# Kernel optimization log

Hardware: AMD Instinct MI355X
Metric: run time of the kernel (lower is better)

Reference implementation:

```python
import jax, jax.numpy as jnp
import numpy as np

# Winograd F(2x2, 3x3) transform matrices
_BT = np.array([[1, 0, -1, 0],
                [0, 1,  1, 0],
                [0, -1, 1, 0],
                [0, 1,  0, -1]], dtype=np.float32)
_G = np.array([[1.0, 0.0, 0.0],
               [0.5, 0.5, 0.5],
               [0.5, -0.5, 0.5],
               [0.0, 0.0, 1.0]], dtype=np.float32)
_AT = np.array([[1, 1, 1, 0],
                [0, 1, -1, -1]], dtype=np.float32)


def setup_inputs() -> dict:
    key = jax.random.key(0)
    k1, k2, k3 = jax.random.split(key, 3)
    B, Cin, Cout, H, W = 16, 128, 256, 64, 64
    X = jax.random.normal(k1, (B, Cin, H, W), dtype=jnp.float32)
    # kaiming-uniform-ish scale for a 3x3 conv
    fan_in = Cin * 9
    bound = 1.0 / np.sqrt(fan_in)
    weight = jax.random.uniform(k2, (Cout, Cin, 3, 3), dtype=jnp.float32,
                                minval=-bound * np.sqrt(3.0), maxval=bound * np.sqrt(3.0))
    bias = jax.random.uniform(k3, (Cout,), dtype=jnp.float32, minval=-bound, maxval=bound)
    return {"X": X, "weight": weight, "bias": bias}


def reference(X, weight, bias):
    # Winograd F(2x2,3x3) convolution, stride 1, padding 1 ('same').
    BT = jnp.asarray(_BT, X.dtype)
    G = jnp.asarray(_G, X.dtype)
    AT = jnp.asarray(_AT, X.dtype)
    Bn, C, H, W = X.shape
    K = weight.shape[0]
    tH, tW = H // 2, W // 2  # number of 2x2 output tiles per dim

    xp = jnp.pad(X, ((0, 0), (0, 0), (1, 1), (1, 1)))
    # overlapping 4x4 input tiles with stride 2 -> [B, C, tH, tW, 4, 4]
    rows = (jnp.arange(tH) * 2)[:, None] + jnp.arange(4)[None, :]  # [tH,4]
    cols = (jnp.arange(tW) * 2)[:, None] + jnp.arange(4)[None, :]  # [tW,4]
    d = xp[:, :, rows[:, None, :, None], cols[None, :, None, :]]   # [B,C,tH,tW,4,4]

    # input transform V = B^T d B
    V = jnp.einsum('px,bcijxy,qy->bcijpq', BT, d, BT)
    # filter transform U = G g G^T -> [K,C,4,4]
    U = jnp.einsum('px,kcxy,qy->kcpq', G, weight, G)
    # elementwise product in transform domain, contracted over input channels
    M = jnp.einsum('kcpq,bcijpq->bkijpq', U, V)
    # inverse transform Y = A^T M A -> 2x2 output tiles
    Y = jnp.einsum('px,bkijxy,qy->bkijpq', AT, M, AT)  # [B,K,tH,tW,2,2]

    out = Y.transpose(0, 1, 2, 4, 3, 5).reshape(Bn, K, H, W)
    return out + bias[None, :, None, None]
```

## Files before the change

kernel.cpp:

```cpp
#include <hip/hip_runtime.h>
#include <hip/hip_bf16.h>
#include <cstdint>

#define CIN   128
#define COUT  256
#define BATCH 16
#define HH    64
#define WW    64
#define TH    32
#define TW    32
#define NT    (BATCH*TH*TW)
#define APQ   (COUT*CIN)
#define BPQ   (NT*CIN)

typedef __bf16 bf16x8 __attribute__((ext_vector_type(8)));
typedef float  f32x4  __attribute__((ext_vector_type(4)));

__device__ __forceinline__ void gload16(const void* g, void* l) {
    __builtin_amdgcn_global_load_lds(
        (const __attribute__((address_space(1))) uint32_t*)g,
        (__attribute__((address_space(3))) uint32_t*)l, 16, 0, 0);
}

__global__ __launch_bounds__(256) void wg_wtrans(const float* __restrict__ w,
                                                 __hip_bfloat16* __restrict__ U) {
    int idx = blockIdx.x * 256 + threadIdx.x;
    if (idx >= COUT * CIN) return;
    const float* wp = w + idx * 9;
    float g[3][3];
#pragma unroll
    for (int x = 0; x < 3; x++)
#pragma unroll
        for (int y = 0; y < 3; y++) g[x][y] = wp[x * 3 + y];

    float t[4][3];
#pragma unroll
    for (int y = 0; y < 3; y++) {
        t[0][y] = g[0][y];
        t[1][y] = 0.5f * (g[0][y] + g[1][y] + g[2][y]);
        t[2][y] = 0.5f * (g[0][y] - g[1][y] + g[2][y]);
        t[3][y] = g[2][y];
    }
#pragma unroll
    for (int p = 0; p < 4; p++) {
        float u0 = t[p][0];
        float u1 = 0.5f * (t[p][0] + t[p][1] + t[p][2]);
        float u2 = 0.5f * (t[p][0] - t[p][1] + t[p][2]);
        float u3 = t[p][2];
        U[(p * 4 + 0) * APQ + idx] = __float2bfloat16(u0);
        U[(p * 4 + 1) * APQ + idx] = __float2bfloat16(u1);
        U[(p * 4 + 2) * APQ + idx] = __float2bfloat16(u2);
        U[(p * 4 + 3) * APQ + idx] = __float2bfloat16(u3);
    }
}

__global__ __launch_bounds__(1024) void wg_itrans(const float* __restrict__ X,
                                                  __hip_bfloat16* __restrict__ V) {
    __shared__ float lds[32 * 265];
    const int c0 = blockIdx.x * 32;
    const int i  = blockIdx.y;
    const int b  = blockIdx.z;
    const int tid = threadIdx.x;

    for (int t = tid; t < 32 * 4; t += 1024) {
        int cc = t >> 2, r = t & 3;
        lds[cc * 265 + r * 66 + 0]  = 0.f;
        lds[cc * 265 + r * 66 + 65] = 0.f;
    }
    for (int t = tid; t < 32 * 4 * 64; t += 1024) {
        int x = t & 63, r = (t >> 6) & 3, cc = t >> 8;
        int y = 2 * i - 1 + r;
        float v = 0.f;
        if (y >= 0 && y < HH) v = X[(((b * CIN) + (c0 + cc)) * HH + y) * WW + x];
        lds[cc * 265 + r * 66 + 1 + x] = v;
    }
    __syncthreads();

    const int c = tid & 31;
    const int j = tid >> 5;
    const float* base = &lds[c * 265 + 2 * j];

    float t0[4], t1[4], t2[4], t3[4];
#pragma unroll
    for (int y = 0; y < 4; y++) {
        float a  = base[0 * 66 + y];
        float bb = base[1 * 66 + y];
        float cc = base[2 * 66 + y];
        float dd = base[3 * 66 + y];
        t0[y] = a - cc;
        t1[y] = bb + cc;
        t2[y] = cc - bb;
        t3[y] = bb - dd;
    }
    float vm[4][4];
#pragma unroll
    for (int p = 0; p < 4; p++) {
        const float* tp = (p == 0) ? t0 : (p == 1) ? t1 : (p == 2) ? t2 : t3;
        vm[p][0] = tp[0] - tp[2];
        vm[p][1] = tp[1] + tp[2];
        vm[p][2] = tp[2] - tp[1];
        vm[p][3] = tp[1] - tp[3];
    }

    const int bij = b * (TH * TW) + i * TW + j;
    const int vo  = bij * CIN + (c0 + c);
#pragma unroll
    for (int p = 0; p < 4; p++)
#pragma unroll
        for (int q = 0; q < 4; q++)
            V[(size_t)(p * 4 + q) * BPQ + vo] = __float2bfloat16(vm[p][q]);
}

#define ABYTES 16384
#define BUFSZ  32768

__global__ __launch_bounds__(512, 2) void wg_gemm13(const __hip_bfloat16* __restrict__ U,
                                                    const __hip_bfloat16* __restrict__ V,
                                                    const float* __restrict__ bias,
                                                    float* __restrict__ out) {
    __shared__ char lds[4 * BUFSZ];

    int orig = blockIdx.x;
    int wgid = (orig & 7) * 32 + (orig >> 3);
    const int mt = wgid & 1, nt = wgid >> 1;
    const int m0 = mt * 128, n0 = nt * 128;

    const int tid  = threadIdx.x;
    const int lane = tid & 63;
    const int wave = tid >> 6;
    const int wm = wave >> 2, wn = wave & 3;

    const __hip_bfloat16* pa[2];
    const __hip_bfloat16* pb[2];
    int ldsA[2], ldsB[2];
#pragma unroll
    for (int ch = 0; ch < 2; ch++) {
        int c = ch * 512 + tid;
        int R = c >> 3;
        int G = (c & 7) ^ (R & 7);
        pa[ch] = U + (m0 + R) * CIN + G * 8;
        pb[ch] = V + (size_t)(n0 + R) * CIN + G * 8;
        ldsA[ch] = c * 16;
        ldsB[ch] = ABYTES + c * 16;
    }

    const int la = lane & 15, hq = lane >> 4, l7 = lane & 7;
    int aoff[2], boff[2];
#pragma unroll
    for (int kk = 0; kk < 2; kk++) {
        int g = (kk * 4 + hq) ^ l7;
        aoff[kk] = (wm * 64 + la) * 128 + (g << 4);
        boff[kk] = ABYTES + (wn * 32 + la) * 128 + (g << 4);
    }

    f32x4 yac[2][2][4][2];
#pragma unroll
    for (int x = 0; x < 2; x++)
#pragma unroll
        for (int y = 0; y < 2; y++)
#pragma unroll
            for (int mi = 0; mi < 4; mi++)
#pragma unroll
                for (int nj = 0; nj < 2; nj++) yac[x][y][mi][nj] = (f32x4){0.f, 0.f, 0.f, 0.f};
    f32x4 mac[4][2];
    const f32x4 fz = (f32x4){0.f, 0.f, 0.f, 0.f};

    bf16x8 aX[4], bX[2], aY[4], bY[2];
    bf16x8 a1[4], b1[2];

    auto stage = [&](int s) {
        char* sb = lds + (s & 3) * BUFSZ;
        const int pq = s >> 1, kb = (s & 1) * 64;
        gload16(pa[0] + pq * APQ + kb, sb + ldsA[0]);
        gload16(pa[1] + pq * APQ + kb, sb + ldsA[1]);
        gload16(pb[0] + (size_t)pq * BPQ + kb, sb + ldsB[0]);
        gload16(pb[1] + (size_t)pq * BPQ + kb, sb + ldsB[1]);
    };

    auto fold = [&](int pq) {
        const int p = pq >> 2, q = pq & 3;
        const float s1p = (p >= 2) ? -1.f : 1.f;
        const float s1q = (q >= 2) ? -1.f : 1.f;
        if (p != 3 && q != 3) {
#pragma unroll
            for (int mi = 0; mi < 4; mi++)
#pragma unroll
                for (int nj = 0; nj < 2; nj++) yac[0][0][mi][nj] += mac[mi][nj];
        }
        if (p != 3 && q != 0) {
#pragma unroll
            for (int mi = 0; mi < 4; mi++)
#pragma unroll
                for (int nj = 0; nj < 2; nj++) yac[0][1][mi][nj] += s1q * mac[mi][nj];
        }
        if (p != 0 && q != 3) {
#pragma unroll
            for (int mi = 0; mi < 4; mi++)
#pragma unroll
                for (int nj = 0; nj < 2; nj++) yac[1][0][mi][nj] += s1p * mac[mi][nj];
        }
        if (p != 0 && q != 0) {
            const float s11 = s1p * s1q;
#pragma unroll
            for (int mi = 0; mi < 4; mi++)
#pragma unroll
                for (int nj = 0; nj < 2; nj++) yac[1][1][mi][nj] += s11 * mac[mi][nj];
        }
    };

#define SLOT(T, AIN, BIN, AOUT, BOUT, VMC, STG, PRE, INIT, LGK2)              \
    {                                                                          \
        const int t_ = (T);                                                    \
        if (STG) stage(t_ + 3);                                                \
        if ((VMC) == 8)      asm volatile("s_waitcnt vmcnt(8)");               \
        else if ((VMC) == 4) asm volatile("s_waitcnt vmcnt(4)");               \
        else if ((VMC) == 0) asm volatile("s_waitcnt vmcnt(0)");               \
        __builtin_amdgcn_s_barrier();                                          \
        __builtin_amdgcn_sched_barrier(0);                                     \
        {                                                                      \
            const char* rb_ = lds + (t_ & 3) * BUFSZ;                          \
            _Pragma("unroll")                                                  \
            for (int mi = 0; mi < 4; mi++)                                     \
                a1[mi] = *reinterpret_cast<const bf16x8*>(rb_ + aoff[1] + mi * 2048); \
            _Pragma("unroll")                                                  \
            for (int nj = 0; nj < 2; nj++)                                     \
                b1[nj] = *reinterpret_cast<const bf16x8*>(rb_ + boff[1] + nj * 2048); \
        }                                                                      \
        __builtin_amdgcn_sched_barrier(0);                                     \
        asm volatile("s_waitcnt lgkmcnt(6)");                                  \
        __builtin_amdgcn_sched_barrier(0);                                     \
        __builtin_amdgcn_s_setprio(1);                                         \
        _Pragma("unroll")                                                      \
        for (int mi = 0; mi < 4; mi++)                                         \
            _Pragma("unroll")                                                  \
            for (int nj = 0; nj < 2; nj++)                                     \
                mac[mi][nj] = __builtin_amdgcn_mfma_f32_16x16x32_bf16(         \
                    AIN[mi], BIN[nj], (INIT) ? fz : mac[mi][nj], 0, 0, 0);     \
        __builtin_amdgcn_s_setprio(0);                                         \
        if (PRE) {                                                             \
            const char* rb2_ = lds + ((t_ + 1) & 3) * BUFSZ;                   \
            _Pragma("unroll")                                                  \
            for (int mi = 0; mi < 4; mi++)                                     \
                AOUT[mi] = *reinterpret_cast<const bf16x8*>(rb2_ + aoff[0] + mi * 2048); \
            _Pragma("unroll")                                                  \
            for (int nj = 0; nj < 2; nj++)                                     \
                BOUT[nj] = *reinterpret_cast<const bf16x8*>(rb2_ + boff[0] + nj * 2048); \
        }                                                                      \
        __builtin_amdgcn_sched_barrier(0);                                     \
        if ((LGK2) == 6) asm volatile("s_waitcnt lgkmcnt(6)");                 \
        else             asm volatile("s_waitcnt lgkmcnt(0)");                 \
        __builtin_amdgcn_sched_barrier(0);                                     \
        __builtin_amdgcn_s_setprio(1);                                         \
        _Pragma("unroll")                                                      \
        for (int mi = 0; mi < 4; mi++)                                         \
            _Pragma("unroll")                                                  \
            for (int nj = 0; nj < 2; nj++)                                     \
                mac[mi][nj] = __builtin_amdgcn_mfma_f32_16x16x32_bf16(         \
                    a1[mi], b1[nj], mac[mi][nj], 0, 0, 0);                     \
        __builtin_amdgcn_s_setprio(0);                                         \
        __builtin_amdgcn_sched_barrier(0);                                     \
        __builtin_amdgcn_s_barrier();                                          \
    }

    stage(0); stage(1); stage(2);
    asm volatile("s_waitcnt vmcnt(8)");
    __builtin_amdgcn_s_barrier();
    {
        const char* rb_ = lds;
#pragma unroll
        for (int mi = 0; mi < 4; mi++)
            aX[mi] = *reinterpret_cast<const bf16x8*>(rb_ + aoff[0] + mi * 2048);
#pragma unroll
        for (int nj = 0; nj < 2; nj++)
            bX[nj] = *reinterpret_cast<const bf16x8*>(rb_ + boff[0] + nj * 2048);
    }

    for (int tt = 0; tt < 28; tt += 2) {
        if (tt >= 2) fold((tt >> 1) - 1);
        SLOT(tt,     aX, bX, aY, bY, 8, true, true, true,  6)
        SLOT(tt + 1, aY, bY, aX, bX, 8, true, true, false, 6)
    }
    fold(13);
    SLOT(28, aX, bX, aY, bY, 8,  true,  true,  true,  6)
    SLOT(29, aY, bY, aX, bX, 4,  false, true,  false, 6)
    fold(14);
    SLOT(30, aX, bX, aY, bY, 0,  false, true,  true,  6)
    SLOT(31, aY, bY, aX, bX, -1, false, false, false, 0)
    fold(15);

#undef SLOT

    const int lr = lane & 15, rg = lane >> 4;
#pragma unroll
    for (int mi = 0; mi < 4; mi++) {
#pragma unroll
        for (int r = 0; r < 4; r++) {
            const int kout = m0 + wm * 64 + mi * 16 + rg * 4 + r;
            const float bvv = bias[kout];
#pragma unroll
            for (int nj = 0; nj < 2; nj++) {
                const int bij = n0 + wn * 32 + nj * 16 + lr;
                const int bb = bij >> 10, ti = (bij >> 5) & 31, tj = bij & 31;
                float* op = out + (((size_t)bb * COUT + kout) * HH + 2 * ti) * WW + 2 * tj;
                *reinterpret_cast<float2*>(op) =
                    make_float2(yac[0][0][mi][nj][r] + bvv, yac[0][1][mi][nj][r] + bvv);
                *reinterpret_cast<float2*>(op + WW) =
                    make_float2(yac[1][0][mi][nj][r] + bvv, yac[1][1][mi][nj][r] + bvv);
            }
        }
    }
}

extern "C" void kernel_launch(void* const* d_in, const int* in_sizes, int n_in,
                              void* d_out, int out_size, void* d_ws, size_t ws_size,
                              hipStream_t stream) {
    const float* X    = (const float*)d_in[0];
    const float* w    = (const float*)d_in[1];
    const float* bias = (const float*)d_in[2];
    float* out        = (float*)d_out;

    __hip_bfloat16* U = (__hip_bfloat16*)d_ws;
    __hip_bfloat16* V = (__hip_bfloat16*)((char*)d_ws + (1u << 20));

    wg_wtrans<<<(COUT * CIN + 255) / 256, 256, 0, stream>>>(w, U);
    wg_itrans<<<dim3(CIN / 32, TH, BATCH), 1024, 0, stream>>>(X, V);
    wg_gemm13<<<(COUT / 128) * (NT / 128), 512, 0, stream>>>(U, V, bias, out);
}
```

Baseline: 68.62 us.

## Shrink GEMM tile to 128x64 with 256 threads and triple-buffered LDS

```diff
diff --git a/kernel.cpp b/kernel.cpp
--- a/kernel.cpp
+++ b/kernel.cpp
@@ -112,35 +112,41 @@
 }
 
 #define ABYTES 16384
-#define BUFSZ  32768
-
-__global__ __launch_bounds__(512, 2) void wg_gemm13(const __hip_bfloat16* __restrict__ U,
+#define BUFSZ  24576
+
+__global__ __launch_bounds__(256, 2) void wg_gemm14(const __hip_bfloat16* __restrict__ U,
                                                     const __hip_bfloat16* __restrict__ V,
                                                     const float* __restrict__ bias,
                                                     float* __restrict__ out) {
-    __shared__ char lds[4 * BUFSZ];
+    __shared__ char lds[3 * BUFSZ];
 
     int orig = blockIdx.x;
-    int wgid = (orig & 7) * 32 + (orig >> 3);
+    int wgid = (orig & 7) * 64 + (orig >> 3);
     const int mt = wgid & 1, nt = wgid >> 1;
-    const int m0 = mt * 128, n0 = nt * 128;
+    const int m0 = mt * 128, n0 = nt * 64;
 
     const int tid  = threadIdx.x;
     const int lane = tid & 63;
     const int wave = tid >> 6;
-    const int wm = wave >> 2, wn = wave & 3;
-
-    const __hip_bfloat16* pa[2];
+    const int wm = wave >> 1, wn = wave & 1;
+
+    const __hip_bfloat16* pa[4];
     const __hip_bfloat16* pb[2];
-    int ldsA[2], ldsB[2];
-#pragma unroll
-    for (int ch = 0; ch < 2; ch++) {
-        int c = ch * 512 + tid;
+    int ldsA[4], ldsB[2];
+#pragma unroll
+    for (int ch = 0; ch < 4; ch++) {
+        int c = ch * 256 + tid;
         int R = c >> 3;
         int G = (c & 7) ^ (R & 7);
         pa[ch] = U + (m0 + R) * CIN + G * 8;
+        ldsA[ch] = c * 16;
+    }
+#pragma unroll
+    for (int ch = 0; ch < 2; ch++) {
+        int c = ch * 256 + tid;
+        int R = c >> 3;
+        int G = (c & 7) ^ (R & 7);
         pb[ch] = V + (size_t)(n0 + R) * CIN + G * 8;
-        ldsA[ch] = c * 16;
         ldsB[ch] = ABYTES + c * 16;
     }
 
@@ -168,11 +174,13 @@
     bf16x8 aX[4], bX[2], aY[4], bY[2];
     bf16x8 a1[4], b1[2];
 
-    auto stage = [&](int s) {
-        char* sb = lds + (s & 3) * BUFSZ;
+    auto stage = [&](int s, int sbuf) {
+        char* sb = lds + sbuf * BUFSZ;
         const int pq = s >> 1, kb = (s & 1) * 64;
         gload16(pa[0] + pq * APQ + kb, sb + ldsA[0]);
         gload16(pa[1] + pq * APQ + kb, sb + ldsA[1]);
+        gload16(pa[2] + pq * APQ + kb, sb + ldsA[2]);
+        gload16(pa[3] + pq * APQ + kb, sb + ldsA[3]);
         gload16(pb[0] + (size_t)pq * BPQ + kb, sb + ldsB[0]);
         gload16(pb[1] + (size_t)pq * BPQ + kb, sb + ldsB[1]);
     };
@@ -208,17 +216,15 @@
         }
     };
 
-#define SLOT(T, AIN, BIN, AOUT, BOUT, VMC, STG, PRE, INIT, LGK2)              \
+#define SLOT(T, BUF, SBUF, PBUF, AIN, BIN, AOUT, BOUT, VMC, STG, PRE, INIT, LGK2) \
     {                                                                          \
-        const int t_ = (T);                                                    \
-        if (STG) stage(t_ + 3);                                                \
-        if ((VMC) == 8)      asm volatile("s_waitcnt vmcnt(8)");               \
-        else if ((VMC) == 4) asm volatile("s_waitcnt vmcnt(4)");               \
+        if (STG) stage((T) + 2, (SBUF));                                       \
+        if ((VMC) == 6)      asm volatile("s_waitcnt vmcnt(6)");               \
         else if ((VMC) == 0) asm volatile("s_waitcnt vmcnt(0)");               \
         __builtin_amdgcn_s_barrier();                                          \
         __builtin_amdgcn_sched_barrier(0);                                     \
         {                                                                      \
-            const char* rb_ = lds + (t_ & 3) * BUFSZ;                          \
+            const char* rb_ = lds + (BUF) * BUFSZ;                             \
             _Pragma("unroll")                                                  \
             for (int mi = 0; mi < 4; mi++)                                     \
                 a1[mi] = *reinterpret_cast<const bf16x8*>(rb_ + aoff[1] + mi * 2048); \
@@ -238,7 +244,7 @@
                     AIN[mi], BIN[nj], (INIT) ? fz : mac[mi][nj], 0, 0, 0);     \
         __builtin_amdgcn_s_setprio(0);                                         \
         if (PRE) {                                                             \
-            const char* rb2_ = lds + ((t_ + 1) & 3) * BUFSZ;                   \
+            const char* rb2_ = lds + (PBUF) * BUFSZ;                           \
             _Pragma("unroll")                                                  \
             for (int mi = 0; mi < 4; mi++)                                     \
                 AOUT[mi] = *reinterpret_cast<const bf16x8*>(rb2_ + aoff[0] + mi * 2048); \
@@ -262,8 +268,9 @@
         __builtin_amdgcn_s_barrier();                                          \
     }
 
-    stage(0); stage(1); stage(2);
-    asm volatile("s_waitcnt vmcnt(8)");
+    stage(0, 0);
+    stage(1, 1);
+    asm volatile("s_waitcnt vmcnt(6)");
     __builtin_amdgcn_s_barrier();
     {
         const char* rb_ = lds;
@@ -275,17 +282,19 @@
             bX[nj] = *reinterpret_cast<const bf16x8*>(rb_ + boff[0] + nj * 2048);
     }
 
-    for (int tt = 0; tt < 28; tt += 2) {
-        if (tt >= 2) fold((tt >> 1) - 1);
-        SLOT(tt,     aX, bX, aY, bY, 8, true, true, true,  6)
-        SLOT(tt + 1, aY, bY, aX, bX, 8, true, true, false, 6)
-    }
-    fold(13);
-    SLOT(28, aX, bX, aY, bY, 8,  true,  true,  true,  6)
-    SLOT(29, aY, bY, aX, bX, 4,  false, true,  false, 6)
-    fold(14);
-    SLOT(30, aX, bX, aY, bY, 0,  false, true,  true,  6)
-    SLOT(31, aY, bY, aX, bX, -1, false, false, false, 0)
+    for (int tt = 0; tt < 30; tt += 6) {
+        SLOT(tt + 0, 0, 2, 1, aX, bX, aY, bY, 6, true, true, true,  6)
+        SLOT(tt + 1, 1, 0, 2, aY, bY, aX, bX, 6, true, true, false, 6)
+        fold(tt >> 1);
+        SLOT(tt + 2, 2, 1, 0, aX, bX, aY, bY, 6, true, true, true,  6)
+        SLOT(tt + 3, 0, 2, 1, aY, bY, aX, bX, 6, true, true, false, 6)
+        fold((tt >> 1) + 1);
+        SLOT(tt + 4, 1, 0, 2, aX, bX, aY, bY, 6, true, true, true,  6)
+        SLOT(tt + 5, 2, 1, 0, aY, bY, aX, bX, 6, true, true, false, 6)
+        fold((tt >> 1) + 2);
+    }
+    SLOT(30, 0, 0, 1, aX, bX, aY, bY, 0, false, true,  true,  6)
+    SLOT(31, 1, 0, 0, aY, bY, aX, bX, -1, false, false, false, 0)
     fold(15);
 
 #undef SLOT
@@ -324,5 +333,5 @@
 
     wg_wtrans<<<(COUT * CIN + 255) / 256, 256, 0, stream>>>(w, U);
     wg_itrans<<<dim3(CIN / 32, TH, BATCH), 1024, 0, stream>>>(X, V);
-    wg_gemm13<<<(COUT / 128) * (NT / 128), 512, 0, stream>>>(U, V, bias, out);
-}
+    wg_gemm14<<<(COUT / 128) * (NT / 64), 256, 0, stream>>>(U, V, bias, out);
+}
```

After: 67.78 us. About the same (-1.2%).

## Restructure input transform: all channels per block, float4 loads, bf16 LDS staging

Applied to the files above, without the earlier changes.

```diff
diff --git a/kernel.cpp b/kernel.cpp
--- a/kernel.cpp
+++ b/kernel.cpp
@@ -54,61 +54,74 @@
     }
 }
 
-__global__ __launch_bounds__(1024) void wg_itrans(const float* __restrict__ X,
-                                                  __hip_bfloat16* __restrict__ V) {
-    __shared__ float lds[32 * 265];
-    const int c0 = blockIdx.x * 32;
-    const int i  = blockIdx.y;
-    const int b  = blockIdx.z;
+__global__ __launch_bounds__(1024) void wg_itrans2(const float* __restrict__ X,
+                                                   __hip_bfloat16* __restrict__ V) {
+    __shared__ __hip_bfloat16 Xp[128 * 266];
+    const int i = blockIdx.x;
+    const int b = blockIdx.y;
     const int tid = threadIdx.x;
 
-    for (int t = tid; t < 32 * 4; t += 1024) {
-        int cc = t >> 2, r = t & 3;
-        lds[cc * 265 + r * 66 + 0]  = 0.f;
-        lds[cc * 265 + r * 66 + 65] = 0.f;
-    }
-    for (int t = tid; t < 32 * 4 * 64; t += 1024) {
-        int x = t & 63, r = (t >> 6) & 3, cc = t >> 8;
+    {
+        int c = tid >> 3, r = (tid >> 1) & 3, e = tid & 1;
+        Xp[c * 266 + r * 66 + e * 65] = __float2bfloat16(0.f);
+    }
+#pragma unroll
+    for (int it = 0; it < 8; ++it) {
+        int flat = it * 4096 + tid * 4;
+        int c = flat >> 8, r = (flat >> 6) & 3, x = flat & 63;
         int y = 2 * i - 1 + r;
-        float v = 0.f;
-        if (y >= 0 && y < HH) v = X[(((b * CIN) + (c0 + cc)) * HH + y) * WW + x];
-        lds[cc * 265 + r * 66 + 1 + x] = v;
+        float4 v = make_float4(0.f, 0.f, 0.f, 0.f);
+        if (y >= 0 && y < HH)
+            v = *reinterpret_cast<const float4*>(&X[(((b * CIN + c) * HH + y) << 6) + x]);
+        int base = c * 266 + r * 66 + 1 + x;
+        Xp[base + 0] = __float2bfloat16(v.x);
+        Xp[base + 1] = __float2bfloat16(v.y);
+        Xp[base + 2] = __float2bfloat16(v.z);
+        Xp[base + 3] = __float2bfloat16(v.w);
     }
     __syncthreads();
 
-    const int c = tid & 31;
-    const int j = tid >> 5;
-    const float* base = &lds[c * 265 + 2 * j];
-
-    float t0[4], t1[4], t2[4], t3[4];
-#pragma unroll
-    for (int y = 0; y < 4; y++) {
-        float a  = base[0 * 66 + y];
-        float bb = base[1 * 66 + y];
-        float cc = base[2 * 66 + y];
-        float dd = base[3 * 66 + y];
-        t0[y] = a - cc;
-        t1[y] = bb + cc;
-        t2[y] = cc - bb;
-        t3[y] = bb - dd;
-    }
-    float vm[4][4];
-#pragma unroll
-    for (int p = 0; p < 4; p++) {
-        const float* tp = (p == 0) ? t0 : (p == 1) ? t1 : (p == 2) ? t2 : t3;
-        vm[p][0] = tp[0] - tp[2];
-        vm[p][1] = tp[1] + tp[2];
-        vm[p][2] = tp[2] - tp[1];
-        vm[p][3] = tp[1] - tp[3];
-    }
-
-    const int bij = b * (TH * TW) + i * TW + j;
-    const int vo  = bij * CIN + (c0 + c);
-#pragma unroll
-    for (int p = 0; p < 4; p++)
-#pragma unroll
-        for (int q = 0; q < 4; q++)
-            V[(size_t)(p * 4 + q) * BPQ + vo] = __float2bfloat16(vm[p][q]);
+    const int c  = tid & 127;
+    const int jj = tid >> 7;
+#pragma unroll
+    for (int jl = 0; jl < 4; ++jl) {
+        const int j = jj * 4 + jl;
+        float d[4][4];
+#pragma unroll
+        for (int r = 0; r < 4; r++) {
+            int off = c * 266 + r * 66 + 2 * j;
+            ushort2 s01 = *reinterpret_cast<const ushort2*>(&Xp[off]);
+            ushort2 s23 = *reinterpret_cast<const ushort2*>(&Xp[off + 2]);
+            d[r][0] = __bfloat162float(*reinterpret_cast<__hip_bfloat16*>(&s01.x));
+            d[r][1] = __bfloat162float(*reinterpret_cast<__hip_bfloat16*>(&s01.y));
+            d[r][2] = __bfloat162float(*reinterpret_cast<__hip_bfloat16*>(&s23.x));
+            d[r][3] = __bfloat162float(*reinterpret_cast<__hip_bfloat16*>(&s23.y));
+        }
+        float t0[4], t1[4], t2[4], t3[4];
+#pragma unroll
+        for (int y = 0; y < 4; y++) {
+            t0[y] = d[0][y] - d[2][y];
+            t1[y] = d[1][y] + d[2][y];
+            t2[y] = d[2][y] - d[1][y];
+            t3[y] = d[1][y] - d[3][y];
+        }
+        float vm[4][4];
+#pragma unroll
+        for (int p = 0; p < 4; p++) {
+            const float* tp = (p == 0) ? t0 : (p == 1) ? t1 : (p == 2) ? t2 : t3;
+            vm[p][0] = tp[0] - tp[2];
+            vm[p][1] = tp[1] + tp[2];
+            vm[p][2] = tp[2] - tp[1];
+            vm[p][3] = tp[1] - tp[3];
+        }
+        const int bij = (b << 10) + (i << 5) + j;
+        const size_t vo = (size_t)bij * CIN + c;
+#pragma unroll
+        for (int p = 0; p < 4; p++)
+#pragma unroll
+            for (int q = 0; q < 4; q++)
+                V[(size_t)(p * 4 + q) * BPQ + vo] = __float2bfloat16(vm[p][q]);
+    }
 }
 
 #define ABYTES 16384
@@ -323,6 +336,6 @@
     __hip_bfloat16* V = (__hip_bfloat16*)((char*)d_ws + (1u << 20));
 
     wg_wtrans<<<(COUT * CIN + 255) / 256, 256, 0, stream>>>(w, U);
-    wg_itrans<<<dim3(CIN / 32, TH, BATCH), 1024, 0, stream>>>(X, V);
+    wg_itrans2<<<dim3(TH, BATCH), 1024, 0, stream>>>(X, V);
     wg_gemm13<<<(COUT / 128) * (NT / 128), 512, 0, stream>>>(U, V, bias, out);
 }
```

New measurement: 67.44 us. Within noise of the previous version (-1.7%).
